# Optimization experiments

Measured on AMD Instinct MI355X. Metric: run time of the kernel, lower is better.

## Reference

```python
import jax, jax.numpy as jnp
import numpy as np

B, N, D, C = 32, 6, 41, 64
FH, FW = 4, 6            # 150//32, 200//32
IN_CH = 768
NX, NY, NZ = 200, 200, 1 # from x/y/zbound
DX = np.array([0.5, 0.5, 20.0], np.float32)
BX = np.array([-49.75, -49.75, 0.0], np.float32)  # bound[0] + step/2


def _frustum():
    # (D, FH, FW, 3) pixel-coord + depth frustum, matching create_frustum
    ds = np.arange(4.0, 45.0, 1.0, dtype=np.float32)             # D = 41
    xs = np.linspace(0.0, 200.0 - 1.0, FW, dtype=np.float32)
    ys = np.linspace(0.0, 150.0 - 1.0, FH, dtype=np.float32)
    g = np.stack(np.broadcast_arrays(xs[None, None, :], ys[None, :, None], ds[:, None, None]), axis=-1)
    return jnp.asarray(g)


def setup_inputs() -> dict:
    key = jax.random.key(0)
    k1, k2, k3 = jax.random.split(key, 3)
    x = jax.random.normal(k1, (B, N, IN_CH, FH, FW), jnp.float32)
    # cam-to-ego base rotation (cam z -> ego x, cam x -> -ego y, cam y -> -ego z)
    R0 = np.array([[0., 0., 1.], [-1., 0., 0.], [0., -1., 0.]], np.float32)
    yaw = 2.0 * np.pi * np.arange(N) / N
    cz, sz = np.cos(yaw).astype(np.float32), np.sin(yaw).astype(np.float32)
    Rz = np.zeros((N, 3, 3), np.float32)
    Rz[:, 0, 0] = cz; Rz[:, 0, 1] = -sz; Rz[:, 1, 0] = sz; Rz[:, 1, 1] = cz; Rz[:, 2, 2] = 1.0
    rots = jnp.asarray(np.broadcast_to((Rz @ R0)[None], (B, N, 3, 3)))
    K = np.array([[100., 0., 100.], [0., 100., 75.], [0., 0., 1.]], np.float32)
    intrins = jnp.asarray(np.broadcast_to(K, (B, N, 3, 3)))
    trans = jax.random.uniform(k2, (B, N, 3), jnp.float32, -2.0, 2.0)
    conv_w = jax.random.normal(k3, (D + C, IN_CH), jnp.float32) * 0.02
    conv_b = jnp.zeros((D + C,), jnp.float32)
    return {"x": x, "rots": rots, "trans": trans, "intrins": intrins, "conv_w": conv_w, "conv_b": conv_b}


def reference(x, rots, trans, intrins, conv_w, conv_b):
    frustum = _frustum()                                        # (D,FH,FW,3)
    # --- get_geometry ---
    pts = jnp.concatenate([frustum[..., :2] * frustum[..., 2:3], frustum[..., 2:3]], -1)
    combine = rots @ jnp.linalg.inv(intrins)                    # (B,N,3,3)
    geom = jnp.einsum('bnij,dhwj->bndhwi', combine, pts) + trans[:, :, None, None, None, :]
    # --- get_cam_feats: 1x1 conv depthnet, softmax depth, outer product ---
    xf = x.reshape(B * N, IN_CH, FH, FW)
    y = jnp.einsum('oc,bchw->bohw', conv_w, xf) + conv_b[None, :, None, None]
    depth_logit = y[:, :D]                                      # (BN,D,FH,FW)
    depth = jax.nn.softmax(depth_logit, axis=1)
    feat = y[:, D:D + C]                                        # (BN,C,FH,FW)
    xv = (depth[:, None] * feat[:, :, None]).reshape(B, N, C, D, FH, FW).transpose(0, 1, 3, 4, 5, 2)
    # --- voxel_pooling: segment-sum over voxel rank, scatter to BEV ---
    xN = xv.reshape(-1, C)                                      # (Nprime, C)
    g = ((geom - (BX - DX / 2.0)) / DX).astype(jnp.int32).reshape(-1, 3)  # trunc like .long()
    Np = xN.shape[0]
    bix = jnp.repeat(jnp.arange(Np // (Np // B) * 0 + B), Np // B)        # batch index per point
    kept = ((g[:, 0] >= 0) & (g[:, 0] < NX) & (g[:, 1] >= 0) & (g[:, 1] < NY)
            & (g[:, 2] >= 0) & (g[:, 2] < NZ))
    idx = ((bix * NZ + g[:, 2]) * NX + g[:, 0]) * NY + g[:, 1]
    idx = jnp.where(kept, idx, 0)
    xm = jnp.where(kept[:, None], xN, 0.0)
    pooled = jax.ops.segment_sum(xm, idx, num_segments=B * NZ * NX * NY)  # (B*NZ*NX*NY, C)
    final = pooled.reshape(B, NZ, NX, NY, C).transpose(0, 1, 4, 2, 3).reshape(B, NZ * C, NX, NY)
    return (final, depth_logit)
```

## Files before the change

### kernel.cpp

```cpp
#include <hip/hip_runtime.h>
#include <hip/hip_bf16.h>

#define B_    32
#define N_    6
#define D_    41
#define C_    64
#define FH_   4
#define FW_   6
#define INCH  768
#define HW    24
#define O_    105
#define PBN   984
#define PPB   5904
#define NPTS  188928
#define FINAL_ELEMS 81920000
#define NSEG  8
#define SEGV  5000
#define NBKT  (B_ * NSEG)


__global__ __launch_bounds__(256) void k_conv_fused(
    const float* __restrict__ x, const float* __restrict__ w,
    const float* __restrict__ bias,
    float* __restrict__ feat_ws, float* __restrict__ depth_ws,
    float* __restrict__ dlogit, int* __restrict__ cnt)
{
    __shared__ float xs[9216];
    __shared__ float ys[O_ * HW];
    __shared__ float smax[HW], srs[HW];

    const int bn = blockIdx.x;
    const int t  = threadIdx.x;
    const int og = t / 6;
    const int q6 = t % 6;

    if (bn == 0) cnt[t] = 0;

    float a[3][4] = {{0.f,0.f,0.f,0.f},{0.f,0.f,0.f,0.f},{0.f,0.f,0.f,0.f}};
    const int o0 = og * 3;
    const float4* wr0 = (const float4*)(w + (size_t)(o0 + 0) * INCH);
    const float4* wr1 = (const float4*)(w + (size_t)(o0 + 1) * INCH);
    const float4* wr2 = (const float4*)(w + (size_t)(o0 + 2) * INCH);
    float4* xs4 = (float4*)xs;

    for (int half = 0; half < 2; ++half) {
        if (half) __syncthreads();
        const float4* xg = (const float4*)(x + (size_t)bn * (INCH * HW)) + half * 2304;
        for (int i = t; i < 2304; i += 256) xs4[i] = xg[i];
        __syncthreads();

        if (t < 210) {
            const int wb = half * 96;
            for (int c4 = 0; c4 < 96; ++c4) {
                float4 w0 = wr0[wb + c4];
                float4 w1 = wr1[wb + c4];
                float4 w2 = wr2[wb + c4];
                int cb = c4 * 4;
                float4 x0 = xs4[(cb + 0) * 6 + q6];
                float4 x1 = xs4[(cb + 1) * 6 + q6];
                float4 x2 = xs4[(cb + 2) * 6 + q6];
                float4 x3 = xs4[(cb + 3) * 6 + q6];
                a[0][0]=fmaf(w0.x,x0.x,a[0][0]); a[0][1]=fmaf(w0.x,x0.y,a[0][1]);
                a[0][2]=fmaf(w0.x,x0.z,a[0][2]); a[0][3]=fmaf(w0.x,x0.w,a[0][3]);
                a[1][0]=fmaf(w1.x,x0.x,a[1][0]); a[1][1]=fmaf(w1.x,x0.y,a[1][1]);
                a[1][2]=fmaf(w1.x,x0.z,a[1][2]); a[1][3]=fmaf(w1.x,x0.w,a[1][3]);
                a[2][0]=fmaf(w2.x,x0.x,a[2][0]); a[2][1]=fmaf(w2.x,x0.y,a[2][1]);
                a[2][2]=fmaf(w2.x,x0.z,a[2][2]); a[2][3]=fmaf(w2.x,x0.w,a[2][3]);
                a[0][0]=fmaf(w0.y,x1.x,a[0][0]); a[0][1]=fmaf(w0.y,x1.y,a[0][1]);
                a[0][2]=fmaf(w0.y,x1.z,a[0][2]); a[0][3]=fmaf(w0.y,x1.w,a[0][3]);
                a[1][0]=fmaf(w1.y,x1.x,a[1][0]); a[1][1]=fmaf(w1.y,x1.y,a[1][1]);
                a[1][2]=fmaf(w1.y,x1.z,a[1][2]); a[1][3]=fmaf(w1.y,x1.w,a[1][3]);
                a[2][0]=fmaf(w2.y,x1.x,a[2][0]); a[2][1]=fmaf(w2.y,x1.y,a[2][1]);
                a[2][2]=fmaf(w2.y,x1.z,a[2][2]); a[2][3]=fmaf(w2.y,x1.w,a[2][3]);
                a[0][0]=fmaf(w0.z,x2.x,a[0][0]); a[0][1]=fmaf(w0.z,x2.y,a[0][1]);
                a[0][2]=fmaf(w0.z,x2.z,a[0][2]); a[0][3]=fmaf(w0.z,x2.w,a[0][3]);
                a[1][0]=fmaf(w1.z,x2.x,a[1][0]); a[1][1]=fmaf(w1.z,x2.y,a[1][1]);
                a[1][2]=fmaf(w1.z,x2.z,a[1][2]); a[1][3]=fmaf(w1.z,x2.w,a[1][3]);
                a[2][0]=fmaf(w2.z,x2.x,a[2][0]); a[2][1]=fmaf(w2.z,x2.y,a[2][1]);
                a[2][2]=fmaf(w2.z,x2.z,a[2][2]); a[2][3]=fmaf(w2.z,x2.w,a[2][3]);
                a[0][0]=fmaf(w0.w,x3.x,a[0][0]); a[0][1]=fmaf(w0.w,x3.y,a[0][1]);
                a[0][2]=fmaf(w0.w,x3.z,a[0][2]); a[0][3]=fmaf(w0.w,x3.w,a[0][3]);
                a[1][0]=fmaf(w1.w,x3.x,a[1][0]); a[1][1]=fmaf(w1.w,x3.y,a[1][1]);
                a[1][2]=fmaf(w1.w,x3.z,a[1][2]); a[1][3]=fmaf(w1.w,x3.w,a[1][3]);
                a[2][0]=fmaf(w2.w,x3.x,a[2][0]); a[2][1]=fmaf(w2.w,x3.y,a[2][1]);
                a[2][2]=fmaf(w2.w,x3.z,a[2][2]); a[2][3]=fmaf(w2.w,x3.w,a[2][3]);
            }
        }
    }

    if (t < 210) {
#pragma unroll
        for (int r = 0; r < 3; r++) {
            float bo = bias[o0 + r];
#pragma unroll
            for (int j = 0; j < 4; j++)
                ys[(o0 + r) * HW + q6 * 4 + j] = a[r][j] + bo;
        }
    }
    __syncthreads();

    if (t < HW) {
        float mx = -1e30f;
        for (int d = 0; d < D_; d++) mx = fmaxf(mx, ys[d * HW + t]);
        float s = 0.f;
        for (int d = 0; d < D_; d++) s = __fadd_rn(s, expf(__fsub_rn(ys[d * HW + t], mx)));
        smax[t] = mx; srs[t] = s;
    }
    __syncthreads();

    for (int u = t; u < D_ * HW; u += 256) {
        float yv = ys[u];
        int hw = u % HW;
        depth_ws[bn * PBN + u] = __fdiv_rn(expf(__fsub_rn(yv, smax[hw])), srs[hw]);
        dlogit[(size_t)bn * PBN + u] = yv;
    }
    for (int u = t; u < C_ * HW; u += 256)
        feat_ws[(size_t)bn * (C_ * HW) + u] = ys[D_ * HW + u];
}

__global__ __launch_bounds__(256) void k_geom(
    const float* __restrict__ m1, const float* __restrict__ trans,
    const float* __restrict__ m2, const float* __restrict__ depth,
    int* __restrict__ cnt, uint2* __restrict__ entries)
{
    __shared__ int lcnt[16], lbase[16];

    const float* rots = (fabsf(m1[0]) > 50.0f) ? m2 : m1;
    const float* intr = (fabsf(m1[0]) > 50.0f) ? m1 : m2;

    int p = blockIdx.x * 256 + threadIdx.x;
    const int t = threadIdx.x;
    if (t < 16) lcnt[t] = 0;
    __syncthreads();

    int b  = p / PPB;
    int pl = p % PPB;
    int n  = pl / PBN;
    int r  = pl % PBN;
    int d  = r / HW;
    int hw = r % HW;
    int h = hw / FW_, wp = hw % FW_;

    float dv = 4.0f + (float)d;
    float xi = (float)((double)wp * (199.0 / 5.0));
    float yi = (float)((double)h  * (149.0 / 3.0));
    float px = __fmul_rn(xi, dv), py = __fmul_rn(yi, dv), pz = dv;

    int bn = b * N_ + n;
    const float* K = intr + bn * 9;
    const float* R = rots + bn * 9;
    const float* T = trans + bn * 3;

    float a00 = K[0], a01 = K[1], a02 = K[2];
    float a11 = K[4], a12 = K[5];
    float a22 = K[8];

    float i00 = __fdiv_rn(1.0f, a00);
    float i11 = __fdiv_rn(1.0f, a11);
    float x0  = __fmul_rn(a01, i00);
    float i01 = __fmul_rn(-i11, x0);
    float i22 = __fdiv_rn(1.0f, a22);
    float y0  = __fmul_rn(a02, i00);
    y0 = __fadd_rn(y0, __fmul_rn(a12, i01));
    float y1  = __fmul_rn(a12, i11);
    float i02 = __fmul_rn(-i22, y0);
    float i12 = __fmul_rn(-i22, y1);
    float i10 = 0.f, i20 = 0.f, i21 = 0.f;

    float r00 = R[0], r01 = R[1], r02 = R[2];
    float r10 = R[3], r11 = R[4], r12 = R[5];
    float r20 = R[6], r21 = R[7], r22 = R[8];

#define MM(u0,u1,u2, v0,v1,v2) \
    __fmaf_rn(u2, v2, __fmaf_rn(u1, v1, __fmul_rn(u0, v0)))
    float c00 = MM(r00, r01, r02, i00, i10, i20);
    float c01 = MM(r00, r01, r02, i01, i11, i21);
    float c02 = MM(r00, r01, r02, i02, i12, i22);
    float c10 = MM(r10, r11, r12, i00, i10, i20);
    float c11 = MM(r10, r11, r12, i01, i11, i21);
    float c12 = MM(r10, r11, r12, i02, i12, i22);
    float c20 = MM(r20, r21, r22, i00, i10, i20);
    float c21 = MM(r20, r21, r22, i01, i11, i21);
    float c22 = MM(r20, r21, r22, i02, i12, i22);
#undef MM

#define DOT3(u0,v0,u1,v1,u2,v2) \
    __fadd_rn(__fadd_rn(__fmul_rn(u0,v0), __fmul_rn(u1,v1)), __fmul_rn(u2,v2))
    float gx = __fadd_rn(DOT3(c00,px, c01,py, c02,pz), T[0]);
    float gy = __fadd_rn(DOT3(c10,px, c11,py, c12,pz), T[1]);
    float gz = __fadd_rn(DOT3(c20,px, c21,py, c22,pz), T[2]);
#undef DOT3

    int ix = (int)__fmul_rn(__fadd_rn(gx, 50.0f), 2.0f);
    int iy = (int)__fmul_rn(__fadd_rn(gy, 50.0f), 2.0f);
    int iz = (int)__fdiv_rn(__fadd_rn(gz, 10.0f), 20.0f);
    bool kept = (ix >= 0) && (ix < 200) && (iy >= 0) && (iy < 200) && (iz == 0);

    const int bmin = (blockIdx.x * 256) / PPB;
    int lb = 0, slot = 0, rel = 0, nhw = 0;
    if (kept) {
        int vl  = ix * 200 + iy;
        int g   = vl / SEGV;
        rel = vl - g * SEGV;
        nhw = n * HW + hw;
        lb  = (b - bmin) * NSEG + g;
        slot = atomicAdd(&lcnt[lb], 1);
    }
    __syncthreads();
    if (t < 16 && lcnt[t] > 0) {
        int gb = (bmin + (t >> 3)) * NSEG + (t & 7);
        lbase[t] = atomicAdd(&cnt[gb], lcnt[t]);
    }
    __syncthreads();
    if (kept) {
        int gb = (bmin + (lb >> 3)) * NSEG + (lb & 7);
        entries[(size_t)gb * PPB + lbase[lb] + slot] =
            make_uint2((unsigned)rel | ((unsigned)nhw << 13),
                       __float_as_uint(depth[p]));
    }
}

__global__ __launch_bounds__(256) void k_splat(
    const float* __restrict__ feat, const int* __restrict__ cnt,
    const uint2* __restrict__ entries, float* __restrict__ out)
{
    __shared__ float plane[SEGV];
    __shared__ float ftab[144];
    int bid = blockIdx.x;
    int b   = bid >> 9;
    int rem = bid & 511;
    int c   = rem >> 3;
    int g   = rem & 7;
    int t   = threadIdx.x;

    float4* pl4 = (float4*)plane;
    for (int i = t; i < SEGV / 4; i += 256) pl4[i] = make_float4(0.f, 0.f, 0.f, 0.f);
    if (t < 144) {
        int n  = t / HW;
        int hw = t - n * HW;
        ftab[t] = feat[(size_t)(b * N_ + n) * (C_ * HW) + c * HW + hw];
    }
    __syncthreads();

    const int bkt = b * NSEG + g;
    const int ne = cnt[bkt];
    const uint2* eb = entries + (size_t)bkt * PPB;
    for (int i = t; i < ne; i += 256) {
        uint2 e = eb[i];
        atomicAdd(&plane[e.x & 8191u], __uint_as_float(e.y) * ftab[e.x >> 13]);
    }
    __syncthreads();

    float4* ob = (float4*)(out + ((size_t)(b * C_ + c) * 40000) + g * SEGV);
    for (int i = t; i < SEGV / 4; i += 256) ob[i] = pl4[i];
}

extern "C" void kernel_launch(void* const* d_in, const int* in_sizes, int n_in,
                              void* d_out, int out_size, void* d_ws, size_t ws_size,
                              hipStream_t stream) {
    const float *x = nullptr, *m1 = nullptr, *m2 = nullptr, *trn = nullptr,
                *w = nullptr, *bias = nullptr;
    for (int i = 0; i < n_in; i++) {
        const float* p = (const float*)d_in[i];
        switch (in_sizes[i]) {
            case 3538944: x = p; break;
            case 1728:    if (!m1) m1 = p; else m2 = p; break;
            case 576:     trn = p; break;
            case 80640:   w = p; break;
            case 105:     bias = p; break;
            default: break;
        }
    }
    if (!x)    x    = (const float*)d_in[0];
    if (!m1)   m1   = (const float*)d_in[1];
    if (!trn)  trn  = (const float*)d_in[2];
    if (!m2)   m2   = (const float*)d_in[3];
    if (!w)    w    = (const float*)d_in[4];
    if (!bias) bias = (const float*)d_in[5];

    float* feat_ws  = (float*)d_ws;
    float* depth_ws = feat_ws + 192 * C_ * HW;
    int*   cnt      = (int*)(depth_ws + NPTS);
    uint2* entries  = (uint2*)(cnt + 256);

    float* out    = (float*)d_out;
    float* dlogit = out + FINAL_ELEMS;

    k_conv_fused<<<192,   256, 0, stream>>>(x, w, bias, feat_ws, depth_ws, dlogit, cnt);
    k_geom      <<<738,   256, 0, stream>>>(m1, trn, m2, depth_ws, cnt, entries);
    k_splat     <<<16384, 256, 0, stream>>>(feat_ws, cnt, entries, out);
}
```

Before: 447.7 us.

## Fuse conv and geometry binning into one launch; pack entries and gather depth in splat

Merges the depthnet conv kernel and the geometry/binning kernel into a single launch. Blocks below 192 run the conv and the remaining blocks run geometry, so the two independent stages overlap. Because the geometry blocks no longer read depth, each entry shrinks from 8 bytes to a 4-byte packed index that also carries the depth bin. The splat kernel then gathers the depth value from the workspace. The counter reset moves to a hipMemsetAsync, which adds an API call, and splat now does an extra indirect load per entry, repeated for every one of the 64 channels.

```diff
diff --git a/kernel.cpp b/kernel.cpp
--- a/kernel.cpp
+++ b/kernel.cpp
@@ -16,120 +16,119 @@
 #define FINAL_ELEMS 81920000
 #define NSEG  8
 #define SEGV  5000
-#define NBKT  (B_ * NSEG)
-
-
-__global__ __launch_bounds__(256) void k_conv_fused(
+#define CONVB 192
+
+
+__global__ __launch_bounds__(256) void k_fused(
     const float* __restrict__ x, const float* __restrict__ w,
     const float* __restrict__ bias,
+    const float* __restrict__ m1, const float* __restrict__ trans,
+    const float* __restrict__ m2,
     float* __restrict__ feat_ws, float* __restrict__ depth_ws,
-    float* __restrict__ dlogit, int* __restrict__ cnt)
+    float* __restrict__ dlogit,
+    int* __restrict__ cnt, unsigned* __restrict__ entries)
 {
     __shared__ float xs[9216];
     __shared__ float ys[O_ * HW];
     __shared__ float smax[HW], srs[HW];
 
-    const int bn = blockIdx.x;
-    const int t  = threadIdx.x;
-    const int og = t / 6;
-    const int q6 = t % 6;
-
-    if (bn == 0) cnt[t] = 0;
-
-    float a[3][4] = {{0.f,0.f,0.f,0.f},{0.f,0.f,0.f,0.f},{0.f,0.f,0.f,0.f}};
-    const int o0 = og * 3;
-    const float4* wr0 = (const float4*)(w + (size_t)(o0 + 0) * INCH);
-    const float4* wr1 = (const float4*)(w + (size_t)(o0 + 1) * INCH);
-    const float4* wr2 = (const float4*)(w + (size_t)(o0 + 2) * INCH);
-    float4* xs4 = (float4*)xs;
-
-    for (int half = 0; half < 2; ++half) {
-        if (half) __syncthreads();
-        const float4* xg = (const float4*)(x + (size_t)bn * (INCH * HW)) + half * 2304;
-        for (int i = t; i < 2304; i += 256) xs4[i] = xg[i];
+    const int t = threadIdx.x;
+
+    if (blockIdx.x < CONVB) {
+        const int bn = blockIdx.x;
+        const int og = t / 6;
+        const int q6 = t % 6;
+
+        float a[3][4] = {{0.f,0.f,0.f,0.f},{0.f,0.f,0.f,0.f},{0.f,0.f,0.f,0.f}};
+        const int o0 = og * 3;
+        const float4* wr0 = (const float4*)(w + (size_t)(o0 + 0) * INCH);
+        const float4* wr1 = (const float4*)(w + (size_t)(o0 + 1) * INCH);
+        const float4* wr2 = (const float4*)(w + (size_t)(o0 + 2) * INCH);
+        float4* xs4 = (float4*)xs;
+
+        for (int half = 0; half < 2; ++half) {
+            if (half) __syncthreads();
+            const float4* xg = (const float4*)(x + (size_t)bn * (INCH * HW)) + half * 2304;
+            for (int i = t; i < 2304; i += 256) xs4[i] = xg[i];
+            __syncthreads();
+
+            if (t < 210) {
+                const int wb = half * 96;
+                for (int c4 = 0; c4 < 96; ++c4) {
+                    float4 w0 = wr0[wb + c4];
+                    float4 w1 = wr1[wb + c4];
+                    float4 w2 = wr2[wb + c4];
+                    int cb = c4 * 4;
+                    float4 x0 = xs4[(cb + 0) * 6 + q6];
+                    float4 x1 = xs4[(cb + 1) * 6 + q6];
+                    float4 x2 = xs4[(cb + 2) * 6 + q6];
+                    float4 x3 = xs4[(cb + 3) * 6 + q6];
+                    a[0][0]=fmaf(w0.x,x0.x,a[0][0]); a[0][1]=fmaf(w0.x,x0.y,a[0][1]);
+                    a[0][2]=fmaf(w0.x,x0.z,a[0][2]); a[0][3]=fmaf(w0.x,x0.w,a[0][3]);
+                    a[1][0]=fmaf(w1.x,x0.x,a[1][0]); a[1][1]=fmaf(w1.x,x0.y,a[1][1]);
+                    a[1][2]=fmaf(w1.x,x0.z,a[1][2]); a[1][3]=fmaf(w1.x,x0.w,a[1][3]);
+                    a[2][0]=fmaf(w2.x,x0.x,a[2][0]); a[2][1]=fmaf(w2.x,x0.y,a[2][1]);
+                    a[2][2]=fmaf(w2.x,x0.z,a[2][2]); a[2][3]=fmaf(w2.x,x0.w,a[2][3]);
+                    a[0][0]=fmaf(w0.y,x1.x,a[0][0]); a[0][1]=fmaf(w0.y,x1.y,a[0][1]);
+                    a[0][2]=fmaf(w0.y,x1.z,a[0][2]); a[0][3]=fmaf(w0.y,x1.w,a[0][3]);
+                    a[1][0]=fmaf(w1.y,x1.x,a[1][0]); a[1][1]=fmaf(w1.y,x1.y,a[1][1]);
+                    a[1][2]=fmaf(w1.y,x1.z,a[1][2]); a[1][3]=fmaf(w1.y,x1.w,a[1][3]);
+                    a[2][0]=fmaf(w2.y,x1.x,a[2][0]); a[2][1]=fmaf(w2.y,x1.y,a[2][1]);
+                    a[2][2]=fmaf(w2.y,x1.z,a[2][2]); a[2][3]=fmaf(w2.y,x1.w,a[2][3]);
+                    a[0][0]=fmaf(w0.z,x2.x,a[0][0]); a[0][1]=fmaf(w0.z,x2.y,a[0][1]);
+                    a[0][2]=fmaf(w0.z,x2.z,a[0][2]); a[0][3]=fmaf(w0.z,x2.w,a[0][3]);
+                    a[1][0]=fmaf(w1.z,x2.x,a[1][0]); a[1][1]=fmaf(w1.z,x2.y,a[1][1]);
+                    a[1][2]=fmaf(w1.z,x2.z,a[1][2]); a[1][3]=fmaf(w1.z,x2.w,a[1][3]);
+                    a[2][0]=fmaf(w2.z,x2.x,a[2][0]); a[2][1]=fmaf(w2.z,x2.y,a[2][1]);
+                    a[2][2]=fmaf(w2.z,x2.z,a[2][2]); a[2][3]=fmaf(w2.z,x2.w,a[2][3]);
+                    a[0][0]=fmaf(w0.w,x3.x,a[0][0]); a[0][1]=fmaf(w0.w,x3.y,a[0][1]);
+                    a[0][2]=fmaf(w0.w,x3.z,a[0][2]); a[0][3]=fmaf(w0.w,x3.w,a[0][3]);
+                    a[1][0]=fmaf(w1.w,x3.x,a[1][0]); a[1][1]=fmaf(w1.w,x3.y,a[1][1]);
+                    a[1][2]=fmaf(w1.w,x3.z,a[1][2]); a[1][3]=fmaf(w1.w,x3.w,a[1][3]);
+                    a[2][0]=fmaf(w2.w,x3.x,a[2][0]); a[2][1]=fmaf(w2.w,x3.y,a[2][1]);
+                    a[2][2]=fmaf(w2.w,x3.z,a[2][2]); a[2][3]=fmaf(w2.w,x3.w,a[2][3]);
+                }
+            }
+        }
+
+        if (t < 210) {
+#pragma unroll
+            for (int r = 0; r < 3; r++) {
+                float bo = bias[o0 + r];
+#pragma unroll
+                for (int j = 0; j < 4; j++)
+                    ys[(o0 + r) * HW + q6 * 4 + j] = a[r][j] + bo;
+            }
+        }
         __syncthreads();
 
-        if (t < 210) {
-            const int wb = half * 96;
-            for (int c4 = 0; c4 < 96; ++c4) {
-                float4 w0 = wr0[wb + c4];
-                float4 w1 = wr1[wb + c4];
-                float4 w2 = wr2[wb + c4];
-                int cb = c4 * 4;
-                float4 x0 = xs4[(cb + 0) * 6 + q6];
-                float4 x1 = xs4[(cb + 1) * 6 + q6];
-                float4 x2 = xs4[(cb + 2) * 6 + q6];
-                float4 x3 = xs4[(cb + 3) * 6 + q6];
-                a[0][0]=fmaf(w0.x,x0.x,a[0][0]); a[0][1]=fmaf(w0.x,x0.y,a[0][1]);
-                a[0][2]=fmaf(w0.x,x0.z,a[0][2]); a[0][3]=fmaf(w0.x,x0.w,a[0][3]);
-                a[1][0]=fmaf(w1.x,x0.x,a[1][0]); a[1][1]=fmaf(w1.x,x0.y,a[1][1]);
-                a[1][2]=fmaf(w1.x,x0.z,a[1][2]); a[1][3]=fmaf(w1.x,x0.w,a[1][3]);
-                a[2][0]=fmaf(w2.x,x0.x,a[2][0]); a[2][1]=fmaf(w2.x,x0.y,a[2][1]);
-                a[2][2]=fmaf(w2.x,x0.z,a[2][2]); a[2][3]=fmaf(w2.x,x0.w,a[2][3]);
-                a[0][0]=fmaf(w0.y,x1.x,a[0][0]); a[0][1]=fmaf(w0.y,x1.y,a[0][1]);
-                a[0][2]=fmaf(w0.y,x1.z,a[0][2]); a[0][3]=fmaf(w0.y,x1.w,a[0][3]);
-                a[1][0]=fmaf(w1.y,x1.x,a[1][0]); a[1][1]=fmaf(w1.y,x1.y,a[1][1]);
-                a[1][2]=fmaf(w1.y,x1.z,a[1][2]); a[1][3]=fmaf(w1.y,x1.w,a[1][3]);
-                a[2][0]=fmaf(w2.y,x1.x,a[2][0]); a[2][1]=fmaf(w2.y,x1.y,a[2][1]);
-                a[2][2]=fmaf(w2.y,x1.z,a[2][2]); a[2][3]=fmaf(w2.y,x1.w,a[2][3]);
-                a[0][0]=fmaf(w0.z,x2.x,a[0][0]); a[0][1]=fmaf(w0.z,x2.y,a[0][1]);
-                a[0][2]=fmaf(w0.z,x2.z,a[0][2]); a[0][3]=fmaf(w0.z,x2.w,a[0][3]);
-                a[1][0]=fmaf(w1.z,x2.x,a[1][0]); a[1][1]=fmaf(w1.z,x2.y,a[1][1]);
-                a[1][2]=fmaf(w1.z,x2.z,a[1][2]); a[1][3]=fmaf(w1.z,x2.w,a[1][3]);
-                a[2][0]=fmaf(w2.z,x2.x,a[2][0]); a[2][1]=fmaf(w2.z,x2.y,a[2][1]);
-                a[2][2]=fmaf(w2.z,x2.z,a[2][2]); a[2][3]=fmaf(w2.z,x2.w,a[2][3]);
-                a[0][0]=fmaf(w0.w,x3.x,a[0][0]); a[0][1]=fmaf(w0.w,x3.y,a[0][1]);
-                a[0][2]=fmaf(w0.w,x3.z,a[0][2]); a[0][3]=fmaf(w0.w,x3.w,a[0][3]);
-                a[1][0]=fmaf(w1.w,x3.x,a[1][0]); a[1][1]=fmaf(w1.w,x3.y,a[1][1]);
-                a[1][2]=fmaf(w1.w,x3.z,a[1][2]); a[1][3]=fmaf(w1.w,x3.w,a[1][3]);
-                a[2][0]=fmaf(w2.w,x3.x,a[2][0]); a[2][1]=fmaf(w2.w,x3.y,a[2][1]);
-                a[2][2]=fmaf(w2.w,x3.z,a[2][2]); a[2][3]=fmaf(w2.w,x3.w,a[2][3]);
-            }
-        }
-    }
-
-    if (t < 210) {
-#pragma unroll
-        for (int r = 0; r < 3; r++) {
-            float bo = bias[o0 + r];
-#pragma unroll
-            for (int j = 0; j < 4; j++)
-                ys[(o0 + r) * HW + q6 * 4 + j] = a[r][j] + bo;
-        }
-    }
-    __syncthreads();
-
-    if (t < HW) {
-        float mx = -1e30f;
-        for (int d = 0; d < D_; d++) mx = fmaxf(mx, ys[d * HW + t]);
-        float s = 0.f;
-        for (int d = 0; d < D_; d++) s = __fadd_rn(s, expf(__fsub_rn(ys[d * HW + t], mx)));
-        smax[t] = mx; srs[t] = s;
-    }
-    __syncthreads();
-
-    for (int u = t; u < D_ * HW; u += 256) {
-        float yv = ys[u];
-        int hw = u % HW;
-        depth_ws[bn * PBN + u] = __fdiv_rn(expf(__fsub_rn(yv, smax[hw])), srs[hw]);
-        dlogit[(size_t)bn * PBN + u] = yv;
-    }
-    for (int u = t; u < C_ * HW; u += 256)
-        feat_ws[(size_t)bn * (C_ * HW) + u] = ys[D_ * HW + u];
-}
-
-__global__ __launch_bounds__(256) void k_geom(
-    const float* __restrict__ m1, const float* __restrict__ trans,
-    const float* __restrict__ m2, const float* __restrict__ depth,
-    int* __restrict__ cnt, uint2* __restrict__ entries)
-{
+        if (t < HW) {
+            float mx = -1e30f;
+            for (int d = 0; d < D_; d++) mx = fmaxf(mx, ys[d * HW + t]);
+            float s = 0.f;
+            for (int d = 0; d < D_; d++) s = __fadd_rn(s, expf(__fsub_rn(ys[d * HW + t], mx)));
+            smax[t] = mx; srs[t] = s;
+        }
+        __syncthreads();
+
+        for (int u = t; u < D_ * HW; u += 256) {
+            float yv = ys[u];
+            int hw = u % HW;
+            depth_ws[bn * PBN + u] = __fdiv_rn(expf(__fsub_rn(yv, smax[hw])), srs[hw]);
+            dlogit[(size_t)bn * PBN + u] = yv;
+        }
+        for (int u = t; u < C_ * HW; u += 256)
+            feat_ws[(size_t)bn * (C_ * HW) + u] = ys[D_ * HW + u];
+        return;
+    }
+
     __shared__ int lcnt[16], lbase[16];
 
     const float* rots = (fabsf(m1[0]) > 50.0f) ? m2 : m1;
     const float* intr = (fabsf(m1[0]) > 50.0f) ? m1 : m2;
 
-    int p = blockIdx.x * 256 + threadIdx.x;
-    const int t = threadIdx.x;
+    const int gb0 = blockIdx.x - CONVB;
+    int p = gb0 * 256 + t;
     if (t < 16) lcnt[t] = 0;
     __syncthreads();
 
@@ -196,33 +195,34 @@
     int iz = (int)__fdiv_rn(__fadd_rn(gz, 10.0f), 20.0f);
     bool kept = (ix >= 0) && (ix < 200) && (iy >= 0) && (iy < 200) && (iz == 0);
 
-    const int bmin = (blockIdx.x * 256) / PPB;
-    int lb = 0, slot = 0, rel = 0, nhw = 0;
+    const int bmin = (gb0 * 256) / PPB;
+    int lb = 0, slot = 0;
+    unsigned epack = 0;
     if (kept) {
         int vl  = ix * 200 + iy;
         int g   = vl / SEGV;
-        rel = vl - g * SEGV;
-        nhw = n * HW + hw;
+        int rel = vl - g * SEGV;
+        int nhw = n * HW + hw;
+        epack = (unsigned)rel | ((unsigned)nhw << 13) | ((unsigned)d << 21);
         lb  = (b - bmin) * NSEG + g;
         slot = atomicAdd(&lcnt[lb], 1);
     }
     __syncthreads();
     if (t < 16 && lcnt[t] > 0) {
-        int gb = (bmin + (t >> 3)) * NSEG + (t & 7);
-        lbase[t] = atomicAdd(&cnt[gb], lcnt[t]);
+        int gbk = (bmin + (t >> 3)) * NSEG + (t & 7);
+        lbase[t] = atomicAdd(&cnt[gbk], lcnt[t]);
     }
     __syncthreads();
     if (kept) {
-        int gb = (bmin + (lb >> 3)) * NSEG + (lb & 7);
-        entries[(size_t)gb * PPB + lbase[lb] + slot] =
-            make_uint2((unsigned)rel | ((unsigned)nhw << 13),
-                       __float_as_uint(depth[p]));
+        int gbk = (bmin + (lb >> 3)) * NSEG + (lb & 7);
+        entries[(size_t)gbk * PPB + lbase[lb] + slot] = epack;
     }
 }
 
 __global__ __launch_bounds__(256) void k_splat(
-    const float* __restrict__ feat, const int* __restrict__ cnt,
-    const uint2* __restrict__ entries, float* __restrict__ out)
+    const float* __restrict__ feat, const float* __restrict__ depth,
+    const int* __restrict__ cnt, const unsigned* __restrict__ entries,
+    float* __restrict__ out)
 {
     __shared__ float plane[SEGV];
     __shared__ float ftab[144];
@@ -232,8 +232,8 @@
     int c   = rem >> 3;
     int g   = rem & 7;
     int t   = threadIdx.x;
-
     float4* pl4 = (float4*)plane;
+
     for (int i = t; i < SEGV / 4; i += 256) pl4[i] = make_float4(0.f, 0.f, 0.f, 0.f);
     if (t < 144) {
         int n  = t / HW;
@@ -244,10 +244,17 @@
 
     const int bkt = b * NSEG + g;
     const int ne = cnt[bkt];
-    const uint2* eb = entries + (size_t)bkt * PPB;
+    const unsigned* eb = entries + (size_t)bkt * PPB;
+    const float* db = depth + (size_t)b * PPB;
     for (int i = t; i < ne; i += 256) {
-        uint2 e = eb[i];
-        atomicAdd(&plane[e.x & 8191u], __uint_as_float(e.y) * ftab[e.x >> 13]);
+        unsigned e = eb[i];
+        int rel = e & 8191u;
+        int nhw = (e >> 13) & 255u;
+        int d   = e >> 21;
+        int n   = nhw / HW;
+        int hw  = nhw - n * HW;
+        float dp = db[n * PBN + d * HW + hw];
+        atomicAdd(&plane[rel], dp * ftab[nhw]);
     }
     __syncthreads();
 
@@ -278,15 +285,17 @@
     if (!w)    w    = (const float*)d_in[4];
     if (!bias) bias = (const float*)d_in[5];
 
-    float* feat_ws  = (float*)d_ws;
-    float* depth_ws = feat_ws + 192 * C_ * HW;
-    int*   cnt      = (int*)(depth_ws + NPTS);
-    uint2* entries  = (uint2*)(cnt + 256);
+    float*    feat_ws  = (float*)d_ws;
+    float*    depth_ws = feat_ws + 192 * C_ * HW;
+    int*      cnt      = (int*)(depth_ws + NPTS);
+    unsigned* entries  = (unsigned*)(cnt + 256);
 
     float* out    = (float*)d_out;
     float* dlogit = out + FINAL_ELEMS;
 
-    k_conv_fused<<<192,   256, 0, stream>>>(x, w, bias, feat_ws, depth_ws, dlogit, cnt);
-    k_geom      <<<738,   256, 0, stream>>>(m1, trn, m2, depth_ws, cnt, entries);
-    k_splat     <<<16384, 256, 0, stream>>>(feat_ws, cnt, entries, out);
+    hipMemsetAsync(cnt, 0, 256 * sizeof(int), stream);
+    k_fused<<<CONVB + 738, 256, 0, stream>>>(x, w, bias, m1, trn, m2,
+                                             feat_ws, depth_ws, dlogit,
+                                             cnt, entries);
+    k_splat<<<16384, 256, 0, stream>>>(feat_ws, depth_ws, cnt, entries, out);
 }
```

After: 449.5 us. No clear change (+0.4%).
